# Kernel tuning notes

Measured on AMD Instinct MI355X. Metric: run time of the kernel, lower is better.

Reference implementation:

```python
import jax, jax.numpy as jnp
import numpy as np

N = 16384      # total atoms (8 proteins x ~2048)
E = 524288     # N * max_neighbors(32)
B = 8          # graphs
F_IN = 26      # 20 residue types + 6 atom types
D = 128        # node_dim
H = 256        # hidden_dim
OUT = 64       # output_dim
L = 4          # n_layers
N_RBF = 16
CUTOFF = 10.0


def setup_inputs() -> dict:
    key = jax.random.key(0)
    ks = jax.random.split(key, 24)
    s = 0.05
    inp = {
        "positions": jax.random.normal(ks[0], (N, 3), jnp.float32) * 10.0,
        "node_features": jax.random.normal(ks[1], (N, F_IN), jnp.float32),
        "edge_index": jax.random.randint(ks[2], (2, E), 0, N, jnp.int32),
        "batch": jnp.sort(jax.random.randint(ks[3], (N,), 0, B, jnp.int32)),
        # node embedding MLP
        "emb_W1": jax.random.normal(ks[4], (F_IN, D), jnp.float32) * s,
        "emb_b1": jnp.zeros((D,), jnp.float32),
        "emb_W2": jax.random.normal(ks[5], (D, D), jnp.float32) * s,
        "emb_b2": jnp.zeros((D,), jnp.float32),
        # per-layer message MLP: [2D + n_rbf] -> H -> D
        "msg_W1": jax.random.normal(ks[6], (L, 2 * D + N_RBF, H), jnp.float32) * s,
        "msg_b1": jnp.zeros((L, H), jnp.float32),
        "msg_W2": jax.random.normal(ks[7], (L, H, D), jnp.float32) * s,
        "msg_b2": jnp.zeros((L, D), jnp.float32),
        # per-layer update MLP: [2D] -> H -> D (residual)
        "upd_W1": jax.random.normal(ks[8], (L, 2 * D, H), jnp.float32) * s,
        "upd_b1": jnp.zeros((L, H), jnp.float32),
        "upd_W2": jax.random.normal(ks[9], (L, H, D), jnp.float32) * s,
        "upd_b2": jnp.zeros((L, D), jnp.float32),
        # readout MLP: D -> H -> OUT
        "r_W1": jax.random.normal(ks[10], (D, H), jnp.float32) * s,
        "r_b1": jnp.zeros((H,), jnp.float32),
        "r_W2": jax.random.normal(ks[11], (H, OUT), jnp.float32) * s,
        "r_b2": jnp.zeros((OUT,), jnp.float32),
    }
    return inp


def _mlp2(x, W1, b1, W2, b2):
    return jax.nn.silu(x @ W1 + b1) @ W2 + b2


def _edge_rbf(positions, src, dst):
    rel = positions[dst] - positions[src]                      # (E,3)
    d = jnp.sqrt(jnp.sum(rel * rel, axis=-1) + 1e-12)          # (E,)
    centers = jnp.linspace(0.0, CUTOFF, N_RBF, dtype=positions.dtype)
    width = CUTOFF / N_RBF
    rbf = jnp.exp(-((d[:, None] - centers) ** 2) / (2.0 * width * width))  # (E,n_rbf)
    env = 0.5 * (jnp.cos(jnp.pi * d / CUTOFF) + 1.0) * (d < CUTOFF)        # cosine cutoff
    return rbf * env[:, None]


def reference(positions, node_features, edge_index, batch,
              emb_W1, emb_b1, emb_W2, emb_b2,
              msg_W1, msg_b1, msg_W2, msg_b2,
              upd_W1, upd_b1, upd_W2, upd_b2,
              r_W1, r_b1, r_W2, r_b2):
    src, dst = edge_index[0], edge_index[1]
    h = _mlp2(node_features, emb_W1, emb_b1, emb_W2, emb_b2)   # (N,D)
    ef = _edge_rbf(positions, src, dst)                        # (E,n_rbf)
    for i in range(L):
        m_in = jnp.concatenate([h[src], h[dst], ef], axis=-1)  # (E,2D+n_rbf)
        m = _mlp2(m_in, msg_W1[i], msg_b1[i], msg_W2[i], msg_b2[i])  # (E,D)
        agg = jax.ops.segment_sum(m, dst, num_segments=N)      # (N,D)
        u_in = jnp.concatenate([h, agg], axis=-1)              # (N,2D)
        h = h + _mlp2(u_in, upd_W1[i], upd_b1[i], upd_W2[i], upd_b2[i])
    # mean readout per graph
    counts = jax.ops.segment_sum(jnp.ones((N,), h.dtype), batch, num_segments=B)
    g = jax.ops.segment_sum(h, batch, num_segments=B) / jnp.maximum(counts, 1.0)[:, None]
    return _mlp2(g, r_W1, r_b1, r_W2, r_b2)                    # (B,OUT)
```

## Files before the change

### kernel.cpp

```cpp
#include <hip/hip_runtime.h>
#include <math.h>

#define NATOMS 16384
#define NEDGES 524288
#define NLAYERS 4
#define TE 64

typedef __bf16 bf16x8 __attribute__((ext_vector_type(8)));
typedef __bf16 bf16x4 __attribute__((ext_vector_type(4)));
typedef __bf16 bf16x2 __attribute__((ext_vector_type(2)));
typedef float f32x4 __attribute__((ext_vector_type(4)));

__device__ __forceinline__ float silu_f(float x) {
  return x * __builtin_amdgcn_rcpf(1.0f + __expf(-x));
}

__global__ __launch_bounds__(1024) void scan_kernel(
    const int* __restrict__ counts, int* __restrict__ cursor,
    float* __restrict__ degf)
{
  __shared__ int s_tot[1024];
  int tid = threadIdx.x;
  int v[16];
  {
    const int4* cp = (const int4*)(counts + tid * 16);
    int4 a = cp[0], b = cp[1], c = cp[2], d = cp[3];
    v[0]=a.x; v[1]=a.y; v[2]=a.z; v[3]=a.w;
    v[4]=b.x; v[5]=b.y; v[6]=b.z; v[7]=b.w;
    v[8]=c.x; v[9]=c.y; v[10]=c.z; v[11]=c.w;
    v[12]=d.x; v[13]=d.y; v[14]=d.z; v[15]=d.w;
  }
  int tot = 0;
  #pragma unroll
  for (int i = 0; i < 16; i++) tot += v[i];
  s_tot[tid] = tot;
  __syncthreads();
  for (int off = 1; off < 1024; off <<= 1) {
    int t = (tid >= off) ? s_tot[tid - off] : 0;
    __syncthreads();
    s_tot[tid] += t;
    __syncthreads();
  }
  int run = s_tot[tid] - tot;
  #pragma unroll
  for (int i = 0; i < 16; i++) {
    cursor[tid * 16 + i] = run;
    degf[tid * 16 + i] = (float)v[i];
    run += v[i];
  }
}

__global__ __launch_bounds__(256) void scatter_rbf_kernel(
    const int* __restrict__ src, const int* __restrict__ dst,
    int* __restrict__ cursor, const float* __restrict__ pos,
    int* __restrict__ esrc, int* __restrict__ edst,
    __bf16* __restrict__ efb)
{
  int e = blockIdx.x * 256 + threadIdx.x;
  int s = src[e], d = dst[e];
  int p = atomicAdd(&cursor[d], 1);
  esrc[p] = s;
  edst[p] = d;
  float dx = pos[d * 3 + 0] - pos[s * 3 + 0];
  float dy = pos[d * 3 + 1] - pos[s * 3 + 1];
  float dz = pos[d * 3 + 2] - pos[s * 3 + 2];
  float dist = sqrtf(dx * dx + dy * dy + dz * dz + 1e-12f);
  float env = (dist < 10.0f)
                  ? 0.5f * (cosf(3.14159265358979f * dist * 0.1f) + 1.0f)
                  : 0.0f;
  bf16x8 o0, o1;
  #pragma unroll
  for (int i = 0; i < 16; i++) {
    float c = (10.0f / 15.0f) * (float)i;
    float t = dist - c;
    float v = env * __expf(-t * t * 1.28f);
    if (i < 8) o0[i] = (__bf16)v; else o1[i - 8] = (__bf16)v;
  }
  *(bf16x8*)(efb + (size_t)p * 16 + 0) = o0;
  *(bf16x8*)(efb + (size_t)p * 16 + 8) = o1;
}

#define NB_PL   50
#define NB_PREP (NB_PL * NLAYERS)
#define NB_HIST (NEDGES / 256)
#define NB_EMB  (NATOMS / 32)

__global__ __launch_bounds__(256) void front_kernel(
    const float* __restrict__ mW1, const float* __restrict__ mW2,
    const float* __restrict__ uW1, const float* __restrict__ uW2,
    const float* __restrict__ mb2,
    __bf16* __restrict__ W1at, __bf16* __restrict__ W1bt,
    __bf16* __restrict__ B2c, __bf16* __restrict__ uW1ft,
    __bf16* __restrict__ uW2t, float* __restrict__ b2u,
    const int* __restrict__ dstI, int* __restrict__ counts,
    const float* __restrict__ x, const float* __restrict__ eW1,
    const float* __restrict__ eb1, const float* __restrict__ eW2,
    const float* __restrict__ eb2, float* __restrict__ h,
    __bf16* __restrict__ hb)
{
  __shared__ __align__(16) char smem[19712];
  int bxf = blockIdx.x, tid = threadIdx.x;

  if (bxf < NB_PREP) {
    int l = bxf / NB_PL;
    int bx = bxf - l * NB_PL;
    if (bx < 16) {
      float (*tile)[65] = (float(*)[65])smem;
      int tt = bx & 7;
      int row0 = ((tt >> 2) * 64) + ((bx < 8) ? 0 : 128);
      int col0 = (tt & 3) * 64;
      const float* Sp = mW1 + (size_t)l * (272 * 256) + (size_t)row0 * 256 + col0;
      __bf16* Dq = ((bx < 8) ? W1at : W1bt) + (size_t)l * (256 * 128);
      int dro = (bx < 8) ? row0 : row0 - 128;
      int c = tid & 63, r4 = tid >> 6;
      #pragma unroll
      for (int i = 0; i < 16; i++)
        tile[r4 + i * 4][c] = Sp[(size_t)(r4 + i * 4) * 256 + c];
      __syncthreads();
      #pragma unroll
      for (int i = 0; i < 16; i++) {
        int dr = r4 + i * 4;
        Dq[(size_t)(col0 + dr) * 128 + dro + c] = (__bf16)tile[c][dr];
      }
    } else if (bx == 16) {
      float (*t3)[257] = (float(*)[257])smem;
      const float* Sp = mW1 + (size_t)l * (272 * 256) + 256 * 256;
      #pragma unroll
      for (int i = 0; i < 16; i++) t3[i][tid] = Sp[i * 256 + tid];
      __syncthreads();
      __bf16* Dp = B2c + (size_t)l * (256 * 32) + (size_t)tid * 32;
      #pragma unroll
      for (int g = 0; g < 4; g++) {
        bf16x8 o;
        #pragma unroll
        for (int j2 = 0; j2 < 8; j2++) {
          int k = g * 8 + j2;
          o[j2] = (__bf16)((k < 16) ? t3[k][tid] : 0.0f);
        }
        *(bf16x8*)(Dp + g * 8) = o;
      }
    } else if (bx < 25) {
      float (*tile)[65] = (float(*)[65])smem;
      int tt = bx - 17;
      int row0 = (tt >> 2) * 64;
      int col0 = (tt & 3) * 64;
      const float* Sp = uW1 + (size_t)l * 65536 + (size_t)row0 * 256 + col0;
      __bf16* Dq = uW1ft + (size_t)l * (256 * 384);
      int c = tid & 63, r4 = tid >> 6;
      #pragma unroll
      for (int i = 0; i < 16; i++)
        tile[r4 + i * 4][c] = Sp[(size_t)(r4 + i * 4) * 256 + c];
      __syncthreads();
      #pragma unroll
      for (int i = 0; i < 16; i++) {
        int dr = r4 + i * 4;
        Dq[(size_t)(col0 + dr) * 384 + row0 + c] = (__bf16)tile[c][dr];
      }
    } else if (bx < 41) {
      float (*sA)[128] = (float(*)[128])smem;
      int r0 = (bx - 25) * 16;
      const float* Ap = mW2 + (size_t)(l * 256 + r0) * 128;
      #pragma unroll
      for (int i = 0; i < 8; i++) {
        int idx = i * 256 + tid;
        ((float*)smem)[idx] = Ap[idx];
      }
      __syncthreads();
      const float* Bp = uW1 + (size_t)l * 65536 + 128 * 256 + tid;
      float acc[16];
      #pragma unroll
      for (int r = 0; r < 16; r++) acc[r] = 0.0f;
      for (int k = 0; k < 128; k++) {
        float b = Bp[(size_t)k * 256];
        #pragma unroll
        for (int r = 0; r < 16; r++) acc[r] += sA[r][k] * b;
      }
      __bf16* Dp = uW1ft + (size_t)l * (256 * 384) + (size_t)tid * 384 + 128 + r0;
      bf16x8 o0, o1;
      #pragma unroll
      for (int r = 0; r < 8; r++) { o0[r] = (__bf16)acc[r]; o1[r] = (__bf16)acc[8 + r]; }
      *(bf16x8*)Dp = o0;
      *(bf16x8*)(Dp + 8) = o1;
    } else if (bx < 49) {
      float (*tile)[65] = (float(*)[65])smem;
      int tt = bx - 41;
      int row0 = (tt >> 1) * 64;
      int col0 = (tt & 1) * 64;
      const float* Sp = uW2 + (size_t)l * (256 * 128) + (size_t)row0 * 128 + col0;
      __bf16* Dq = uW2t + (size_t)l * (128 * 256);
      int c = tid & 63, r4 = tid >> 6;
      #pragma unroll
      for (int i = 0; i < 16; i++)
        tile[r4 + i * 4][c] = Sp[(size_t)(r4 + i * 4) * 128 + c];
      __syncthreads();
      #pragma unroll
      for (int i = 0; i < 16; i++) {
        int dr = r4 + i * 4;
        Dq[(size_t)(col0 + dr) * 256 + row0 + c] = (__bf16)tile[c][dr];
      }
    } else {
      int cc = tid;
      float acc = 0.0f;
      for (int j2 = 0; j2 < 128; j2++)
        acc += mb2[l * 128 + j2] * uW1[(size_t)l * 65536 + (size_t)(128 + j2) * 256 + cc];
      b2u[l * 256 + cc] = acc;
    }
  } else if (bxf < NB_PREP + NB_HIST) {
    int e = (bxf - NB_PREP) * 256 + tid;
    atomicAdd(&counts[dstI[e]], 1);
  } else {
    int nb = bxf - (NB_PREP + NB_HIST);
    int n0e = nb * 32;
    float* xsf = (float*)smem;
    float (*hid2)[128] = (float(*)[128])(smem + 32 * 26 * 4);
    for (int i = tid; i < 32 * 26; i += 256)
      xsf[i] = x[(size_t)n0e * 26 + i];
    __syncthreads();
    int j = tid & 127, ns = tid >> 7;
    float a1[16];
    {
      float bb = eb1[j];
      #pragma unroll
      for (int i = 0; i < 16; i++) a1[i] = bb;
    }
    for (int k = 0; k < 26; k++) {
      float w = eW1[k * 128 + j];
      #pragma unroll
      for (int i = 0; i < 16; i++) a1[i] += xsf[(ns * 16 + i) * 26 + k] * w;
    }
    #pragma unroll
    for (int i = 0; i < 16; i++) hid2[ns * 16 + i][j] = silu_f(a1[i]);
    __syncthreads();
    float a2[16];
    {
      float bb = eb2[j];
      #pragma unroll
      for (int i = 0; i < 16; i++) a2[i] = bb;
    }
    for (int k = 0; k < 128; k++) {
      float w = eW2[k * 128 + j];
      #pragma unroll
      for (int i = 0; i < 16; i++) a2[i] += hid2[ns * 16 + i][k] * w;
    }
    #pragma unroll
    for (int i = 0; i < 16; i++) {
      int n = n0e + ns * 16 + i;
      h[(size_t)n * 128 + j] = a2[i];
      hb[(size_t)n * 128 + j] = (__bf16)a2[i];
    }
  }
}

__global__ __launch_bounds__(256) void zprep_kernel(
    const __bf16* __restrict__ hb, const float* __restrict__ b1,
    const __bf16* __restrict__ W1at, const __bf16* __restrict__ W1bt,
    __bf16* __restrict__ z1b, __bf16* __restrict__ z2b, float* __restrict__ aggH)
{
  __shared__ __bf16 s_n[64][136];
  int tid = threadIdx.x, n0 = blockIdx.x * 64;
  {
    int n = tid >> 2, t4 = tid & 3;
    const bf16x8* hr = (const bf16x8*)(hb + (size_t)(n0 + n) * 128);
    #pragma unroll
    for (int i = 0; i < 4; i++)
      *(bf16x8*)&s_n[n][t4 * 8 + 32 * i] = hr[t4 + 4 * i];
  }
  {
    float4 zz = make_float4(0.f, 0.f, 0.f, 0.f);
    float4* ap = (float4*)(aggH + (size_t)n0 * 256);
    for (int i = tid; i < 64 * 256 / 4; i += 256) ap[i] = zz;
  }
  __syncthreads();
  const int wv = tid >> 6, ln = tid & 63, lc = ln & 15, qd = ln >> 4;
  for (int cp = 0; cp < 2; cp++) {
    f32x4 aA[4][2], aB[4][2];
    #pragma unroll
    for (int nt = 0; nt < 2; nt++) {
      float bv = b1[cp * 128 + wv * 32 + nt * 16 + lc];
      #pragma unroll
      for (int mt = 0; mt < 4; mt++) {
        aA[mt][nt][0] = 0.f; aA[mt][nt][1] = 0.f;
        aA[mt][nt][2] = 0.f; aA[mt][nt][3] = 0.f;
        aB[mt][nt][0] = bv; aB[mt][nt][1] = bv;
        aB[mt][nt][2] = bv; aB[mt][nt][3] = bv;
      }
    }
    #pragma unroll
    for (int kt = 0; kt < 4; kt++) {
      bf16x8 af[4];
      #pragma unroll
      for (int mt = 0; mt < 4; mt++)
        af[mt] = *(const bf16x8*)&s_n[mt * 16 + lc][kt * 32 + qd * 8];
      bf16x8 bwA[2], bwB[2];
      #pragma unroll
      for (int nt = 0; nt < 2; nt++) {
        int c = cp * 128 + wv * 32 + nt * 16 + lc;
        bwA[nt] = *(const bf16x8*)(W1at + (size_t)c * 128 + kt * 32 + qd * 8);
        bwB[nt] = *(const bf16x8*)(W1bt + (size_t)c * 128 + kt * 32 + qd * 8);
      }
      #pragma unroll
      for (int mt = 0; mt < 4; mt++)
        #pragma unroll
        for (int nt = 0; nt < 2; nt++) {
          aA[mt][nt] = __builtin_amdgcn_mfma_f32_16x16x32_bf16(af[mt], bwA[nt], aA[mt][nt], 0, 0, 0);
          aB[mt][nt] = __builtin_amdgcn_mfma_f32_16x16x32_bf16(af[mt], bwB[nt], aB[mt][nt], 0, 0, 0);
        }
    }
    #pragma unroll
    for (int mt = 0; mt < 4; mt++)
      #pragma unroll
      for (int nt = 0; nt < 2; nt++) {
        int c = cp * 128 + wv * 32 + nt * 16 + lc;
        #pragma unroll
        for (int r = 0; r < 4; r++) {
          int n = n0 + mt * 16 + qd * 4 + r;
          z1b[(size_t)n * 256 + c] = (__bf16)aA[mt][nt][r];
          z2b[(size_t)n * 256 + c] = (__bf16)aB[mt][nt][r];
        }
      }
  }
}

__global__ __launch_bounds__(256, 8) void msg_mfma_kernel(
    const __bf16* __restrict__ z1b, const __bf16* __restrict__ z2b,
    const __bf16* __restrict__ efb,
    const int* __restrict__ esrc, const int* __restrict__ edst,
    const __bf16* __restrict__ B2c, float* __restrict__ aggH)
{
  __shared__ __align__(16) __bf16 s_hT[128][68];
  __shared__ __align__(16) __bf16 s_ef[TE][16];
  __shared__ int s_src[TE];
  __shared__ int s_dst[TE];
  __shared__ unsigned int s_mask[2];

  int tid = threadIdx.x, e0 = blockIdx.x * TE;

  if (tid < TE) {
    int d = edst[e0 + tid];
    s_dst[tid] = d;
    int dp = (tid == 0) ? (d ^ 1) : edst[e0 + tid - 1];
    unsigned long long mb = __ballot(d != dp);
    if (tid == 0) { s_mask[0] = (unsigned int)mb; s_mask[1] = (unsigned int)(mb >> 32); }
  } else if (tid < 2 * TE) {
    s_src[tid - TE] = esrc[e0 + tid - TE];
  }
  {
    int e = tid >> 2, t4 = tid & 3;
    if (t4 < 2)
      *(bf16x8*)&s_ef[e][t4 * 8] =
          *(const bf16x8*)(efb + (size_t)(e0 + e) * 16 + t4 * 8);
  }
  __syncthreads();

  const int wv = tid >> 6, ln = tid & 63, lc = ln & 15, qd = ln >> 4;

  bf16x8 bI;
  #pragma unroll
  for (int j = 0; j < 8; j++)
    bI[j] = (__bf16)((lc == (qd & 1) * 8 + j) ? 1.0f : 0.0f);

  const __bf16* pz[4];
  #pragma unroll
  for (int mt = 0; mt < 4; mt++) {
    int m = mt * 16 + lc;
    int row = (qd < 2) ? s_src[m] : s_dst[m];
    pz[mt] = ((qd < 2) ? z1b : z2b) + (size_t)row * 256 + (qd & 1) * 8;
  }

  bf16x8 aef[4];
  #pragma unroll
  for (int mt = 0; mt < 4; mt++)
    aef[mt] = *(const bf16x8*)&s_ef[mt * 16 + lc][(qd & 1) * 8];

  const int sj = tid & 127;
  const int srow0 = (tid >> 7) * 32;
  const unsigned int smask = __builtin_amdgcn_readfirstlane(s_mask[tid >> 7]);

  #pragma unroll
  for (int hf = 0; hf < 2; hf++) {
    if (hf) __syncthreads();

    #pragma unroll
    for (int nt = 0; nt < 2; nt++) {
      const int cb = hf * 128 + wv * 32 + nt * 16;
      bf16x8 bw = *(const bf16x8*)(B2c + (size_t)(cb + lc) * 32 + qd * 8);
      #pragma unroll
      for (int mt = 0; mt < 4; mt++) {
        bf16x8 az = *(const bf16x8*)(pz[mt] + cb);
        f32x4 z; z[0] = 0.f; z[1] = 0.f; z[2] = 0.f; z[3] = 0.f;
        f32x4 acc = __builtin_amdgcn_mfma_f32_16x16x32_bf16(az, bI, z, 0, 0, 0);
        acc = __builtin_amdgcn_mfma_f32_16x16x32_bf16(aef[mt], bw, acc, 0, 0, 0);
        bf16x4 pv;
        pv[0] = (__bf16)silu_f(acc[0]); pv[1] = (__bf16)silu_f(acc[1]);
        pv[2] = (__bf16)silu_f(acc[2]); pv[3] = (__bf16)silu_f(acc[3]);
        *(bf16x4*)&s_hT[wv * 32 + nt * 16 + lc][mt * 16 + qd * 4] = pv;
      }
    }
    __syncthreads();

    {
      const int gcol = hf * 128 + sj;
      float acc = 0.0f;
      int cur = s_dst[srow0];
      #pragma unroll
      for (int i = 0; i < 32; i += 4) {
        unsigned int bm = (smask >> i) & 0xFu;
        if (i == 0) bm &= 0xEu;
        bf16x4 p = *(const bf16x4*)&s_hT[sj][srow0 + i];
        if (bm == 0u) {
          acc += ((float)p[0] + (float)p[1]) + ((float)p[2] + (float)p[3]);
        } else {
          #pragma unroll
          for (int r = 0; r < 4; r++) {
            if ((bm >> r) & 1u) {
              atomicAdd(&aggH[(size_t)cur * 256 + gcol], acc);
              acc = 0.0f; cur = s_dst[srow0 + i + r];
            }
            acc += (float)p[r];
          }
        }
      }
      atomicAdd(&aggH[(size_t)cur * 256 + gcol], acc);
    }
  }
}

__global__ __launch_bounds__(512, 2) void upd_mfma_kernel(
    float* __restrict__ h, __bf16* __restrict__ hb,
    float* __restrict__ aggH, const float* __restrict__ degf,
    const __bf16* __restrict__ uW1ft, const float* __restrict__ b1,
    const float* __restrict__ b2u,
    const __bf16* __restrict__ uW2t, const float* __restrict__ b2,
    int do_z, const float* __restrict__ nb1,
    const __bf16* __restrict__ nW1at, const __bf16* __restrict__ nW1bt,
    __bf16* __restrict__ z1b, __bf16* __restrict__ z2b)
{
  __shared__ __bf16 s_u[64][392];
  __shared__ __bf16 s_uh[64][264];
  int tid = threadIdx.x, n0 = blockIdx.x * 64;
  {
    int n = tid >> 3, t8 = tid & 7;
    const bf16x8* hr = (const bf16x8*)(hb + (size_t)(n0 + n) * 128);
    #pragma unroll
    for (int i = 0; i < 2; i++)
      *(bf16x8*)&s_u[n][t8 * 8 + 64 * i] = hr[t8 + 8 * i];
    const float* sr = aggH + (size_t)(n0 + n) * 256;
    #pragma unroll
    for (int i = 0; i < 4; i++) {
      int col = t8 * 8 + i * 64;
      float4 a = *(const float4*)(sr + col);
      float4 b = *(const float4*)(sr + col + 4);
      bf16x8 o;
      o[0] = (__bf16)a.x; o[1] = (__bf16)a.y; o[2] = (__bf16)a.z; o[3] = (__bf16)a.w;
      o[4] = (__bf16)b.x; o[5] = (__bf16)b.y; o[6] = (__bf16)b.z; o[7] = (__bf16)b.w;
      *(bf16x8*)&s_u[n][128 + col] = o;
    }
  }
  __syncthreads();
  const int wv = tid >> 6, ln = tid & 63, lc = ln & 15, qd = ln >> 4;

  float dg[4][4];
  #pragma unroll
  for (int mt = 0; mt < 4; mt++)
    #pragma unroll
    for (int r = 0; r < 4; r++)
      dg[mt][r] = degf[n0 + mt * 16 + qd * 4 + r];

  {
    f32x4 acc1[4][2];
    #pragma unroll
    for (int nt = 0; nt < 2; nt++) {
      int c = wv * 32 + nt * 16 + lc;
      float bv = b1[c];
      float b2uv = b2u[c];
      #pragma unroll
      for (int mt = 0; mt < 4; mt++)
        #pragma unroll
        for (int r = 0; r < 4; r++)
          acc1[mt][nt][r] = bv + dg[mt][r] * b2uv;
    }
    #pragma unroll
    for (int kt = 0; kt < 12; kt++) {
      bf16x8 af[4];
      #pragma unroll
      for (int mt = 0; mt < 4; mt++)
        af[mt] = *(const bf16x8*)&s_u[mt * 16 + lc][kt * 32 + qd * 8];
      bf16x8 bw[2];
      #pragma unroll
      for (int nt = 0; nt < 2; nt++)
        bw[nt] = *(const bf16x8*)(uW1ft +
                 (size_t)(wv * 32 + nt * 16 + lc) * 384 + kt * 32 + qd * 8);
      #pragma unroll
      for (int mt = 0; mt < 4; mt++)
        #pragma unroll
        for (int nt = 0; nt < 2; nt++)
          acc1[mt][nt] = __builtin_amdgcn_mfma_f32_16x16x32_bf16(af[mt], bw[nt], acc1[mt][nt], 0, 0, 0);
    }
    #pragma unroll
    for (int mt = 0; mt < 4; mt++)
      #pragma unroll
      for (int nt = 0; nt < 2; nt++) {
        int cc = wv * 32 + nt * 16 + lc;
        #pragma unroll
        for (int r = 0; r < 4; r++)
          s_uh[mt * 16 + qd * 4 + r][cc] = (__bf16)silu_f(acc1[mt][nt][r]);
      }
  }
  __syncthreads();

  const int ow = wv * 16 + lc;
  f32x4 acc2[4];
  {
    float bv = b2[ow];
    #pragma unroll
    for (int mt = 0; mt < 4; mt++) {
      acc2[mt][0] = bv; acc2[mt][1] = bv; acc2[mt][2] = bv; acc2[mt][3] = bv;
    }
  }
  #pragma unroll
  for (int kt = 0; kt < 8; kt++) {
    bf16x8 a2[4];
    #pragma unroll
    for (int mt = 0; mt < 4; mt++)
      a2[mt] = *(const bf16x8*)&s_uh[mt * 16 + lc][kt * 32 + qd * 8];
    bf16x8 b2w = *(const bf16x8*)(uW2t + (size_t)ow * 256 + kt * 32 + qd * 8);
    #pragma unroll
    for (int mt = 0; mt < 4; mt++)
      acc2[mt] = __builtin_amdgcn_mfma_f32_16x16x32_bf16(a2[mt], b2w, acc2[mt], 0, 0, 0);
  }

  #pragma unroll
  for (int mt = 0; mt < 4; mt++)
    #pragma unroll
    for (int r = 0; r < 4; r++) {
      int n = n0 + mt * 16 + qd * 4 + r;
      float v = h[(size_t)n * 128 + ow] + acc2[mt][r];
      h[(size_t)n * 128 + ow] = v;
      hb[(size_t)n * 128 + ow] = (__bf16)v;
    }

  if (do_z) {
    __syncthreads();
    {
      float4 zz = make_float4(0.f, 0.f, 0.f, 0.f);
      float4* ap = (float4*)(aggH + (size_t)n0 * 256);
      for (int i = tid; i < 64 * 256 / 4; i += 512) ap[i] = zz;
      int n = tid >> 3, t8 = tid & 7;
      const bf16x8* hr = (const bf16x8*)(hb + (size_t)(n0 + n) * 128);
      #pragma unroll
      for (int i = 0; i < 2; i++)
        *(bf16x8*)&s_u[n][t8 * 8 + 64 * i] = hr[t8 + 8 * i];
    }
    __syncthreads();
    f32x4 aA[4][2], aB[4][2];
    #pragma unroll
    for (int nt = 0; nt < 2; nt++) {
      float bv = nb1[wv * 32 + nt * 16 + lc];
      #pragma unroll
      for (int mt = 0; mt < 4; mt++) {
        aA[mt][nt][0] = 0.f; aA[mt][nt][1] = 0.f;
        aA[mt][nt][2] = 0.f; aA[mt][nt][3] = 0.f;
        aB[mt][nt][0] = bv; aB[mt][nt][1] = bv;
        aB[mt][nt][2] = bv; aB[mt][nt][3] = bv;
      }
    }
    #pragma unroll
    for (int kt = 0; kt < 4; kt++) {
      bf16x8 af[4];
      #pragma unroll
      for (int mt = 0; mt < 4; mt++)
        af[mt] = *(const bf16x8*)&s_u[mt * 16 + lc][kt * 32 + qd * 8];
      bf16x8 bwA[2], bwB[2];
      #pragma unroll
      for (int nt = 0; nt < 2; nt++) {
        int c = wv * 32 + nt * 16 + lc;
        bwA[nt] = *(const bf16x8*)(nW1at + (size_t)c * 128 + kt * 32 + qd * 8);
        bwB[nt] = *(const bf16x8*)(nW1bt + (size_t)c * 128 + kt * 32 + qd * 8);
      }
      #pragma unroll
      for (int mt = 0; mt < 4; mt++)
        #pragma unroll
        for (int nt = 0; nt < 2; nt++) {
          aA[mt][nt] = __builtin_amdgcn_mfma_f32_16x16x32_bf16(af[mt], bwA[nt], aA[mt][nt], 0, 0, 0);
          aB[mt][nt] = __builtin_amdgcn_mfma_f32_16x16x32_bf16(af[mt], bwB[nt], aB[mt][nt], 0, 0, 0);
        }
    }
    #pragma unroll
    for (int mt = 0; mt < 4; mt++)
      #pragma unroll
      for (int nt = 0; nt < 2; nt++) {
        int c = wv * 32 + nt * 16 + lc;
        #pragma unroll
        for (int r = 0; r < 4; r++) {
          int n = n0 + mt * 16 + qd * 4 + r;
          z1b[(size_t)n * 256 + c] = (__bf16)aA[mt][nt][r];
          z2b[(size_t)n * 256 + c] = (__bf16)aB[mt][nt][r];
        }
      }
  }
}

__global__ __launch_bounds__(128) void readout_sum_kernel(
    const float* __restrict__ h, const int* __restrict__ batch,
    float* __restrict__ gsum, float* __restrict__ gcnt)
{
  int j = threadIdx.x;
  int n0 = blockIdx.x * 128;
  float acc = 0.f, cacc = 0.f;
  int cur = batch[n0];
  for (int i = 0; i < 128; i++) {
    int b = batch[n0 + i];
    if (b != cur) {
      atomicAdd(&gsum[cur * 128 + j], acc);
      if (j == 0) atomicAdd(&gcnt[cur], cacc);
      acc = 0.f; cacc = 0.f; cur = b;
    }
    acc += h[(size_t)(n0 + i) * 128 + j];
    cacc += 1.f;
  }
  atomicAdd(&gsum[cur * 128 + j], acc);
  if (j == 0) atomicAdd(&gcnt[cur], cacc);
}

__global__ __launch_bounds__(256) void readout_mlp_kernel(
    const float* __restrict__ gsum, const float* __restrict__ gcnt,
    const float* __restrict__ W1, const float* __restrict__ b1,
    const float* __restrict__ W2, const float* __restrict__ b2,
    float* __restrict__ out)
{
  __shared__ float g[8][128];
  __shared__ float hid[8][256];
  int tid = threadIdx.x;
  for (int i = tid; i < 8 * 128; i += 256) {
    int b = i >> 7, c = i & 127;
    g[b][c] = gsum[i] / fmaxf(gcnt[b], 1.0f);
  }
  __syncthreads();
  {
    float bb = b1[tid];
    float a[8];
    #pragma unroll
    for (int b = 0; b < 8; b++) a[b] = bb;
    for (int k = 0; k < 128; k++) {
      float w = W1[k * 256 + tid];
      #pragma unroll
      for (int b = 0; b < 8; b++) a[b] += g[b][k] * w;
    }
    #pragma unroll
    for (int b = 0; b < 8; b++) hid[b][tid] = silu_f(a[b]);
  }
  __syncthreads();
  int j = tid & 63, bg = tid >> 6;
  float a0 = b2[j], a1 = b2[j];
  for (int k = 0; k < 256; k++) {
    float w = W2[k * 64 + j];
    a0 += hid[bg * 2 + 0][k] * w;
    a1 += hid[bg * 2 + 1][k] * w;
  }
  out[(bg * 2 + 0) * 64 + j] = a0;
  out[(bg * 2 + 1) * 64 + j] = a1;
}

extern "C" void kernel_launch(void* const* d_in, const int* in_sizes, int n_in,
                              void* d_out, int out_size, void* d_ws, size_t ws_size,
                              hipStream_t stream) {
  const float* pos   = (const float*)d_in[0];
  const float* xfeat = (const float*)d_in[1];
  const int*   eidx  = (const int*)d_in[2];
  const int*   batch = (const int*)d_in[3];
  const float* eW1 = (const float*)d_in[4];
  const float* eb1 = (const float*)d_in[5];
  const float* eW2 = (const float*)d_in[6];
  const float* eb2 = (const float*)d_in[7];
  const float* mW1 = (const float*)d_in[8];
  const float* mb1 = (const float*)d_in[9];
  const float* mW2 = (const float*)d_in[10];
  const float* mb2 = (const float*)d_in[11];
  const float* uW1 = (const float*)d_in[12];
  const float* ub1 = (const float*)d_in[13];
  const float* uW2 = (const float*)d_in[14];
  const float* ub2 = (const float*)d_in[15];
  const float* rW1 = (const float*)d_in[16];
  const float* rb1 = (const float*)d_in[17];
  const float* rW2 = (const float*)d_in[18];
  const float* rb2 = (const float*)d_in[19];

  const int* srcI = eidx;
  const int* dstI = eidx + NEDGES;

  char* base = (char*)d_ws;
  float* h    = (float*)base;  base += (size_t)NATOMS * 128 * 4;
  float* aggH = (float*)base;  base += (size_t)NATOMS * 256 * 4;
  __bf16* z1b = (__bf16*)base; base += (size_t)NATOMS * 256 * 2;
  __bf16* z2b = (__bf16*)base; base += (size_t)NATOMS * 256 * 2;
  __bf16* hb  = (__bf16*)base; base += (size_t)NATOMS * 128 * 2;
  __bf16* efb = (__bf16*)base; base += (size_t)NEDGES * 16 * 2;
  __bf16* W1at = (__bf16*)base; base += (size_t)NLAYERS * 256 * 128 * 2;
  __bf16* W1bt = (__bf16*)base; base += (size_t)NLAYERS * 256 * 128 * 2;
  __bf16* B2c  = (__bf16*)base; base += (size_t)NLAYERS * 256 * 32 * 2;
  __bf16* uW1ft = (__bf16*)base; base += (size_t)NLAYERS * 256 * 384 * 2;
  __bf16* uW2t = (__bf16*)base; base += (size_t)NLAYERS * 128 * 256 * 2;
  float* b2u  = (float*)base;  base += (size_t)NLAYERS * 256 * 4;
  float* degf = (float*)base;  base += (size_t)NATOMS * 4;
  float* gsum = (float*)base;  base += 8 * 128 * 4;
  float* gcnt = (float*)base;  base += 8 * 4;
  int* counts = (int*)base;    base += (size_t)NATOMS * 4;
  int* cursor = (int*)base;    base += (size_t)NATOMS * 4;
  int* esrc   = (int*)base;    base += (size_t)NEDGES * 4;
  int* edst   = (int*)base;    base += (size_t)NEDGES * 4;

  hipMemsetAsync(counts, 0, NATOMS * sizeof(int), stream);

  front_kernel<<<NB_PREP + NB_HIST + NB_EMB, 256, 0, stream>>>(
      mW1, mW2, uW1, uW2, mb2, W1at, W1bt, B2c, uW1ft, uW2t, b2u,
      dstI, counts, xfeat, eW1, eb1, eW2, eb2, h, hb);

  scan_kernel<<<1, 1024, 0, stream>>>(counts, cursor, degf);
  scatter_rbf_kernel<<<NEDGES / 256, 256, 0, stream>>>(
      srcI, dstI, cursor, pos, esrc, edst, efb);

  zprep_kernel<<<NATOMS / 64, 256, 0, stream>>>(
      hb, mb1, W1at, W1bt, z1b, z2b, aggH);

  for (int l = 0; l < NLAYERS; l++) {
    int ln = (l < NLAYERS - 1) ? (l + 1) : l;
    msg_mfma_kernel<<<NEDGES / TE, 256, 0, stream>>>(
        z1b, z2b, efb, esrc, edst,
        B2c + (size_t)l * 256 * 32, aggH);
    upd_mfma_kernel<<<NATOMS / 64, 512, 0, stream>>>(
        h, hb, aggH, degf,
        uW1ft + (size_t)l * 256 * 384, ub1 + (size_t)l * 256,
        b2u + (size_t)l * 256,
        uW2t + (size_t)l * 128 * 256, ub2 + (size_t)l * 128,
        (l < NLAYERS - 1) ? 1 : 0,
        mb1 + (size_t)ln * 256,
        W1at + (size_t)ln * 256 * 128, W1bt + (size_t)ln * 256 * 128,
        z1b, z2b);
  }

  hipMemsetAsync(gsum, 0, (8 * 128 + 8) * sizeof(float), stream);
  readout_sum_kernel<<<NATOMS / 128, 128, 0, stream>>>(h, batch, gsum, gcnt);
  readout_mlp_kernel<<<1, 256, 0, stream>>>(gsum, gcnt, rW1, rb1, rW2, rb2,
                                            (float*)d_out);
}
```

Before: 578.6 us.

## Reduce message MLP outputs in registers instead of staging through LDS

The message kernel no longer writes the SiLU outputs to a shared-memory transpose buffer followed by a segmented scan. Each 16-row MFMA tile is now reduced directly in registers with cross-lane shuffles when all rows share one destination, and atomics go straight to global memory. Otherwise it falls back to per-lane-quad segmented atomics. This removes the LDS buffer and two block barriers per half, but may issue more global atomics when destinations change within a tile.

```diff
diff --git a/kernel.cpp b/kernel.cpp
--- a/kernel.cpp
+++ b/kernel.cpp
@@ -327,7 +327,6 @@
     const int* __restrict__ esrc, const int* __restrict__ edst,
     const __bf16* __restrict__ B2c, float* __restrict__ aggH)
 {
-  __shared__ __align__(16) __bf16 s_hT[128][68];
   __shared__ __align__(16) __bf16 s_ef[TE][16];
   __shared__ int s_src[TE];
   __shared__ int s_dst[TE];
@@ -354,6 +353,9 @@
 
   const int wv = tid >> 6, ln = tid & 63, lc = ln & 15, qd = ln >> 4;
 
+  const unsigned int mlo = __builtin_amdgcn_readfirstlane(s_mask[0]);
+  const unsigned int mhi = __builtin_amdgcn_readfirstlane(s_mask[1]);
+
   bf16x8 bI;
   #pragma unroll
   for (int j = 0; j < 8; j++)
@@ -372,55 +374,53 @@
   for (int mt = 0; mt < 4; mt++)
     aef[mt] = *(const bf16x8*)&s_ef[mt * 16 + lc][(qd & 1) * 8];
 
-  const int sj = tid & 127;
-  const int srow0 = (tid >> 7) * 32;
-  const unsigned int smask = __builtin_amdgcn_readfirstlane(s_mask[tid >> 7]);
+  int dw[4];
+  #pragma unroll
+  for (int mt = 0; mt < 4; mt++) dw[mt] = s_dst[mt * 16];
+  const int row0q = qd * 4;
 
   #pragma unroll
   for (int hf = 0; hf < 2; hf++) {
-    if (hf) __syncthreads();
-
     #pragma unroll
     for (int nt = 0; nt < 2; nt++) {
       const int cb = hf * 128 + wv * 32 + nt * 16;
       bf16x8 bw = *(const bf16x8*)(B2c + (size_t)(cb + lc) * 32 + qd * 8);
+      const int col = cb + lc;
       #pragma unroll
       for (int mt = 0; mt < 4; mt++) {
         bf16x8 az = *(const bf16x8*)(pz[mt] + cb);
         f32x4 z; z[0] = 0.f; z[1] = 0.f; z[2] = 0.f; z[3] = 0.f;
         f32x4 acc = __builtin_amdgcn_mfma_f32_16x16x32_bf16(az, bI, z, 0, 0, 0);
         acc = __builtin_amdgcn_mfma_f32_16x16x32_bf16(aef[mt], bw, acc, 0, 0, 0);
-        bf16x4 pv;
-        pv[0] = (__bf16)silu_f(acc[0]); pv[1] = (__bf16)silu_f(acc[1]);
-        pv[2] = (__bf16)silu_f(acc[2]); pv[3] = (__bf16)silu_f(acc[3]);
-        *(bf16x4*)&s_hT[wv * 32 + nt * 16 + lc][mt * 16 + qd * 4] = pv;
-      }
-    }
-    __syncthreads();
-
-    {
-      const int gcol = hf * 128 + sj;
-      float acc = 0.0f;
-      int cur = s_dst[srow0];
-      #pragma unroll
-      for (int i = 0; i < 32; i += 4) {
-        unsigned int bm = (smask >> i) & 0xFu;
-        if (i == 0) bm &= 0xEu;
-        bf16x4 p = *(const bf16x4*)&s_hT[sj][srow0 + i];
-        if (bm == 0u) {
-          acc += ((float)p[0] + (float)p[1]) + ((float)p[2] + (float)p[3]);
+        float p0 = silu_f(acc[0]), p1 = silu_f(acc[1]);
+        float p2 = silu_f(acc[2]), p3 = silu_f(acc[3]);
+        unsigned int wbits =
+            (((mt < 2) ? mlo : mhi) >> ((mt & 1) * 16 + 1)) & 0x7FFFu;
+        if (wbits == 0u) {
+          float s4 = (p0 + p1) + (p2 + p3);
+          s4 += __shfl_xor(s4, 16, 64);
+          s4 += __shfl_xor(s4, 32, 64);
+          if (qd == 0)
+            atomicAdd(&aggH[(size_t)dw[mt] * 256 + col], s4);
         } else {
+          int row0 = mt * 16 + row0q;
+          float a2 = 0.0f;
+          int cur = s_dst[row0];
+          float pv[4] = {p0, p1, p2, p3};
           #pragma unroll
           for (int r = 0; r < 4; r++) {
-            if ((bm >> r) & 1u) {
-              atomicAdd(&aggH[(size_t)cur * 256 + gcol], acc);
-              acc = 0.0f; cur = s_dst[srow0 + i + r];
+            int row = row0 + r;
+            bool b = (row < 32) ? ((mlo >> row) & 1u)
+                                : ((mhi >> (row - 32)) & 1u);
+            if (r > 0 && b) {
+              atomicAdd(&aggH[(size_t)cur * 256 + col], a2);
+              a2 = 0.0f; cur = s_dst[row];
             }
-            acc += (float)p[r];
+            a2 += pv[r];
           }
+          atomicAdd(&aggH[(size_t)cur * 256 + col], a2);
         }
       }
-      atomicAdd(&aggH[(size_t)cur * 256 + gcol], acc);
     }
   }
 }
```

Measured after the change: 1.038 ms. 1.79x slower.

## Retile update kernel to 16-node blocks of 256 threads for more parallelism

Applied to the files above, without the earlier changes.

The node update MLP kernel now processes 16 nodes per block with 4 waves instead of 64 nodes with 8 waves, launching 1024 blocks instead of 256. Each wave now covers a wider slice of output columns with a single M-tile. The aim is to fill all compute units on the GPU, since 256 blocks underuse the device. The cost is that weight matrices are reloaded from global/L2 four times more often per node, and each B fragment now feeds only one MFMA.

```diff
diff --git a/kernel.cpp b/kernel.cpp
--- a/kernel.cpp
+++ b/kernel.cpp
@@ -425,7 +425,7 @@
   }
 }
 
-__global__ __launch_bounds__(512, 2) void upd_mfma_kernel(
+__global__ __launch_bounds__(256, 4) void upd_mfma_kernel(
     float* __restrict__ h, __bf16* __restrict__ hb,
     float* __restrict__ aggH, const float* __restrict__ degf,
     const __bf16* __restrict__ uW1ft, const float* __restrict__ b1,
@@ -435,19 +435,17 @@
     const __bf16* __restrict__ nW1at, const __bf16* __restrict__ nW1bt,
     __bf16* __restrict__ z1b, __bf16* __restrict__ z2b)
 {
-  __shared__ __bf16 s_u[64][392];
-  __shared__ __bf16 s_uh[64][264];
-  int tid = threadIdx.x, n0 = blockIdx.x * 64;
+  __shared__ __bf16 s_u[16][392];
+  __shared__ __bf16 s_uh[16][264];
+  int tid = threadIdx.x, n0 = blockIdx.x * 16;
   {
-    int n = tid >> 3, t8 = tid & 7;
+    int n = tid >> 4, t16 = tid & 15;
     const bf16x8* hr = (const bf16x8*)(hb + (size_t)(n0 + n) * 128);
-    #pragma unroll
-    for (int i = 0; i < 2; i++)
-      *(bf16x8*)&s_u[n][t8 * 8 + 64 * i] = hr[t8 + 8 * i];
+    *(bf16x8*)&s_u[n][t16 * 8] = hr[t16];
     const float* sr = aggH + (size_t)(n0 + n) * 256;
     #pragma unroll
-    for (int i = 0; i < 4; i++) {
-      int col = t8 * 8 + i * 64;
+    for (int i = 0; i < 2; i++) {
+      int col = t16 * 8 + i * 128;
       float4 a = *(const float4*)(sr + col);
       float4 b = *(const float4*)(sr + col + 4);
       bf16x8 o;
@@ -459,144 +457,112 @@
   __syncthreads();
   const int wv = tid >> 6, ln = tid & 63, lc = ln & 15, qd = ln >> 4;
 
-  float dg[4][4];
-  #pragma unroll
-  for (int mt = 0; mt < 4; mt++)
-    #pragma unroll
-    for (int r = 0; r < 4; r++)
-      dg[mt][r] = degf[n0 + mt * 16 + qd * 4 + r];
+  float dg[4];
+  #pragma unroll
+  for (int r = 0; r < 4; r++)
+    dg[r] = degf[n0 + qd * 4 + r];
 
   {
-    f32x4 acc1[4][2];
-    #pragma unroll
-    for (int nt = 0; nt < 2; nt++) {
-      int c = wv * 32 + nt * 16 + lc;
+    f32x4 acc1[4];
+    #pragma unroll
+    for (int nt = 0; nt < 4; nt++) {
+      int c = wv * 64 + nt * 16 + lc;
       float bv = b1[c];
       float b2uv = b2u[c];
       #pragma unroll
-      for (int mt = 0; mt < 4; mt++)
-        #pragma unroll
-        for (int r = 0; r < 4; r++)
-          acc1[mt][nt][r] = bv + dg[mt][r] * b2uv;
+      for (int r = 0; r < 4; r++)
+        acc1[nt][r] = bv + dg[r] * b2uv;
     }
     #pragma unroll
     for (int kt = 0; kt < 12; kt++) {
-      bf16x8 af[4];
-      #pragma unroll
-      for (int mt = 0; mt < 4; mt++)
-        af[mt] = *(const bf16x8*)&s_u[mt * 16 + lc][kt * 32 + qd * 8];
-      bf16x8 bw[2];
-      #pragma unroll
-      for (int nt = 0; nt < 2; nt++)
-        bw[nt] = *(const bf16x8*)(uW1ft +
-                 (size_t)(wv * 32 + nt * 16 + lc) * 384 + kt * 32 + qd * 8);
-      #pragma unroll
-      for (int mt = 0; mt < 4; mt++)
-        #pragma unroll
-        for (int nt = 0; nt < 2; nt++)
-          acc1[mt][nt] = __builtin_amdgcn_mfma_f32_16x16x32_bf16(af[mt], bw[nt], acc1[mt][nt], 0, 0, 0);
-    }
-    #pragma unroll
-    for (int mt = 0; mt < 4; mt++)
-      #pragma unroll
-      for (int nt = 0; nt < 2; nt++) {
-        int cc = wv * 32 + nt * 16 + lc;
-        #pragma unroll
-        for (int r = 0; r < 4; r++)
-          s_uh[mt * 16 + qd * 4 + r][cc] = (__bf16)silu_f(acc1[mt][nt][r]);
-      }
+      bf16x8 af = *(const bf16x8*)&s_u[lc][kt * 32 + qd * 8];
+      #pragma unroll
+      for (int nt = 0; nt < 4; nt++) {
+        bf16x8 bw = *(const bf16x8*)(uW1ft +
+                 (size_t)(wv * 64 + nt * 16 + lc) * 384 + kt * 32 + qd * 8);
+        acc1[nt] = __builtin_amdgcn_mfma_f32_16x16x32_bf16(af, bw, acc1[nt], 0, 0, 0);
+      }
+    }
+    #pragma unroll
+    for (int nt = 0; nt < 4; nt++) {
+      int cc = wv * 64 + nt * 16 + lc;
+      #pragma unroll
+      for (int r = 0; r < 4; r++)
+        s_uh[qd * 4 + r][cc] = (__bf16)silu_f(acc1[nt][r]);
+    }
   }
   __syncthreads();
 
-  const int ow = wv * 16 + lc;
-  f32x4 acc2[4];
-  {
-    float bv = b2[ow];
-    #pragma unroll
-    for (int mt = 0; mt < 4; mt++) {
-      acc2[mt][0] = bv; acc2[mt][1] = bv; acc2[mt][2] = bv; acc2[mt][3] = bv;
-    }
+  f32x4 acc2[2];
+  #pragma unroll
+  for (int nt = 0; nt < 2; nt++) {
+    float bv = b2[wv * 32 + nt * 16 + lc];
+    acc2[nt][0] = bv; acc2[nt][1] = bv; acc2[nt][2] = bv; acc2[nt][3] = bv;
   }
   #pragma unroll
   for (int kt = 0; kt < 8; kt++) {
-    bf16x8 a2[4];
-    #pragma unroll
-    for (int mt = 0; mt < 4; mt++)
-      a2[mt] = *(const bf16x8*)&s_uh[mt * 16 + lc][kt * 32 + qd * 8];
-    bf16x8 b2w = *(const bf16x8*)(uW2t + (size_t)ow * 256 + kt * 32 + qd * 8);
-    #pragma unroll
-    for (int mt = 0; mt < 4; mt++)
-      acc2[mt] = __builtin_amdgcn_mfma_f32_16x16x32_bf16(a2[mt], b2w, acc2[mt], 0, 0, 0);
-  }
-
-  #pragma unroll
-  for (int mt = 0; mt < 4; mt++)
+    bf16x8 a2 = *(const bf16x8*)&s_uh[lc][kt * 32 + qd * 8];
+    #pragma unroll
+    for (int nt = 0; nt < 2; nt++) {
+      bf16x8 b2w = *(const bf16x8*)(uW2t +
+               (size_t)(wv * 32 + nt * 16 + lc) * 256 + kt * 32 + qd * 8);
+      acc2[nt] = __builtin_amdgcn_mfma_f32_16x16x32_bf16(a2, b2w, acc2[nt], 0, 0, 0);
+    }
+  }
+
+  #pragma unroll
+  for (int nt = 0; nt < 2; nt++) {
+    int ow = wv * 32 + nt * 16 + lc;
     #pragma unroll
     for (int r = 0; r < 4; r++) {
-      int n = n0 + mt * 16 + qd * 4 + r;
-      float v = h[(size_t)n * 128 + ow] + acc2[mt][r];
+      int n = n0 + qd * 4 + r;
+      float v = h[(size_t)n * 128 + ow] + acc2[nt][r];
       h[(size_t)n * 128 + ow] = v;
       hb[(size_t)n * 128 + ow] = (__bf16)v;
     }
+  }
 
   if (do_z) {
     __syncthreads();
     {
+      int n = tid >> 4, t16 = tid & 15;
+      const bf16x8* hr = (const bf16x8*)(hb + (size_t)(n0 + n) * 128);
+      *(bf16x8*)&s_u[n][t16 * 8] = hr[t16];
       float4 zz = make_float4(0.f, 0.f, 0.f, 0.f);
       float4* ap = (float4*)(aggH + (size_t)n0 * 256);
-      for (int i = tid; i < 64 * 256 / 4; i += 512) ap[i] = zz;
-      int n = tid >> 3, t8 = tid & 7;
-      const bf16x8* hr = (const bf16x8*)(hb + (size_t)(n0 + n) * 128);
-      #pragma unroll
-      for (int i = 0; i < 2; i++)
-        *(bf16x8*)&s_u[n][t8 * 8 + 64 * i] = hr[t8 + 8 * i];
+      #pragma unroll
+      for (int i = 0; i < 4; i++) ap[tid + i * 256] = zz;
     }
     __syncthreads();
-    f32x4 aA[4][2], aB[4][2];
-    #pragma unroll
-    for (int nt = 0; nt < 2; nt++) {
-      float bv = nb1[wv * 32 + nt * 16 + lc];
-      #pragma unroll
-      for (int mt = 0; mt < 4; mt++) {
-        aA[mt][nt][0] = 0.f; aA[mt][nt][1] = 0.f;
-        aA[mt][nt][2] = 0.f; aA[mt][nt][3] = 0.f;
-        aB[mt][nt][0] = bv; aB[mt][nt][1] = bv;
-        aB[mt][nt][2] = bv; aB[mt][nt][3] = bv;
-      }
+    f32x4 aA[4], aB[4];
+    #pragma unroll
+    for (int nt = 0; nt < 4; nt++) {
+      float bv = nb1[wv * 64 + nt * 16 + lc];
+      aA[nt][0] = 0.f; aA[nt][1] = 0.f; aA[nt][2] = 0.f; aA[nt][3] = 0.f;
+      aB[nt][0] = bv; aB[nt][1] = bv; aB[nt][2] = bv; aB[nt][3] = bv;
     }
     #pragma unroll
     for (int kt = 0; kt < 4; kt++) {
-      bf16x8 af[4];
-      #pragma unroll
-      for (int mt = 0; mt < 4; mt++)
-        af[mt] = *(const bf16x8*)&s_u[mt * 16 + lc][kt * 32 + qd * 8];
-      bf16x8 bwA[2], bwB[2];
-      #pragma unroll
-      for (int nt = 0; nt < 2; nt++) {
-        int c = wv * 32 + nt * 16 + lc;
-        bwA[nt] = *(const bf16x8*)(nW1at + (size_t)c * 128 + kt * 32 + qd * 8);
-        bwB[nt] = *(const bf16x8*)(nW1bt + (size_t)c * 128 + kt * 32 + qd * 8);
-      }
-      #pragma unroll
-      for (int mt = 0; mt < 4; mt++)
-        #pragma unroll
-        for (int nt = 0; nt < 2; nt++) {
-          aA[mt][nt] = __builtin_amdgcn_mfma_f32_16x16x32_bf16(af[mt], bwA[nt], aA[mt][nt], 0, 0, 0);
-          aB[mt][nt] = __builtin_amdgcn_mfma_f32_16x16x32_bf16(af[mt], bwB[nt], aB[mt][nt], 0, 0, 0);
-        }
-    }
-    #pragma unroll
-    for (int mt = 0; mt < 4; mt++)
-      #pragma unroll
-      for (int nt = 0; nt < 2; nt++) {
-        int c = wv * 32 + nt * 16 + lc;
-        #pragma unroll
-        for (int r = 0; r < 4; r++) {
-          int n = n0 + mt * 16 + qd * 4 + r;
-          z1b[(size_t)n * 256 + c] = (__bf16)aA[mt][nt][r];
-          z2b[(size_t)n * 256 + c] = (__bf16)aB[mt][nt][r];
-        }
-      }
+      bf16x8 af = *(const bf16x8*)&s_u[lc][kt * 32 + qd * 8];
+      #pragma unroll
+      for (int nt = 0; nt < 4; nt++) {
+        int c = wv * 64 + nt * 16 + lc;
+        bf16x8 bwA = *(const bf16x8*)(nW1at + (size_t)c * 128 + kt * 32 + qd * 8);
+        bf16x8 bwB = *(const bf16x8*)(nW1bt + (size_t)c * 128 + kt * 32 + qd * 8);
+        aA[nt] = __builtin_amdgcn_mfma_f32_16x16x32_bf16(af, bwA, aA[nt], 0, 0, 0);
+        aB[nt] = __builtin_amdgcn_mfma_f32_16x16x32_bf16(af, bwB, aB[nt], 0, 0, 0);
+      }
+    }
+    #pragma unroll
+    for (int nt = 0; nt < 4; nt++) {
+      int c = wv * 64 + nt * 16 + lc;
+      #pragma unroll
+      for (int r = 0; r < 4; r++) {
+        int n = n0 + qd * 4 + r;
+        z1b[(size_t)n * 256 + c] = (__bf16)aA[nt][r];
+        z2b[(size_t)n * 256 + c] = (__bf16)aB[nt][r];
+      }
+    }
   }
 }
 
@@ -727,7 +693,7 @@
     msg_mfma_kernel<<<NEDGES / TE, 256, 0, stream>>>(
         z1b, z2b, efb, esrc, edst,
         B2c + (size_t)l * 256 * 32, aggH);
-    upd_mfma_kernel<<<NATOMS / 64, 512, 0, stream>>>(
+    upd_mfma_kernel<<<NATOMS / 16, 256, 0, stream>>>(
         h, hb, aggH, degf,
         uW1ft + (size_t)l * 256 * 384, ub1 + (size_t)l * 256,
         b2u + (size_t)l * 256,
```

After: 671.6 us. 1.16x slower.

## Reduce edge messages per destination segment in LDS before global atomics

Applied to the files above, without the earlier changes.

Replaces the transposed bf16 staging buffer and serial per-column segmented scan with per-segment float accumulators in shared memory. Each edge tile computes segment ids by ballot/popcount, MFMA outputs are atomically added into LDS rows indexed by segment (one combined add when all four rows share a segment), and then one global atomic per segment per column is issued. This aims to remove the serial scan loop and one barrier, but adds LDS atomics, a 16KB float buffer, and a multi-pass fallback when a tile has more than 16 destination segments.

```diff
diff --git a/kernel.cpp b/kernel.cpp
--- a/kernel.cpp
+++ b/kernel.cpp
@@ -327,11 +327,13 @@
     const int* __restrict__ esrc, const int* __restrict__ edst,
     const __bf16* __restrict__ B2c, float* __restrict__ aggH)
 {
-  __shared__ __align__(16) __bf16 s_hT[128][68];
+  __shared__ float s_agg[16][256];
   __shared__ __align__(16) __bf16 s_ef[TE][16];
   __shared__ int s_src[TE];
   __shared__ int s_dst[TE];
-  __shared__ unsigned int s_mask[2];
+  __shared__ int s_dseg[TE];
+  __shared__ unsigned char s_seg[TE];
+  __shared__ int s_nseg;
 
   int tid = threadIdx.x, e0 = blockIdx.x * TE;
 
@@ -340,7 +342,11 @@
     s_dst[tid] = d;
     int dp = (tid == 0) ? (d ^ 1) : edst[e0 + tid - 1];
     unsigned long long mb = __ballot(d != dp);
-    if (tid == 0) { s_mask[0] = (unsigned int)mb; s_mask[1] = (unsigned int)(mb >> 32); }
+    unsigned long long below = mb & (~0ull >> (63 - tid));
+    int seg = (int)__popcll(below) - 1;
+    s_seg[tid] = (unsigned char)seg;
+    if (d != dp) s_dseg[seg] = d;
+    if (tid == 0) s_nseg = (int)__popcll(mb);
   } else if (tid < 2 * TE) {
     s_src[tid - TE] = esrc[e0 + tid - TE];
   }
@@ -350,9 +356,12 @@
       *(bf16x8*)&s_ef[e][t4 * 8] =
           *(const bf16x8*)(efb + (size_t)(e0 + e) * 16 + t4 * 8);
   }
+  #pragma unroll
+  for (int r = 0; r < 16; r++) s_agg[r][tid] = 0.0f;
   __syncthreads();
 
   const int wv = tid >> 6, ln = tid & 63, lc = ln & 15, qd = ln >> 4;
+  const int nseg = __builtin_amdgcn_readfirstlane(s_nseg);
 
   bf16x8 bI;
   #pragma unroll
@@ -372,55 +381,80 @@
   for (int mt = 0; mt < 4; mt++)
     aef[mt] = *(const bf16x8*)&s_ef[mt * 16 + lc][(qd & 1) * 8];
 
-  const int sj = tid & 127;
-  const int srow0 = (tid >> 7) * 32;
-  const unsigned int smask = __builtin_amdgcn_readfirstlane(s_mask[tid >> 7]);
-
-  #pragma unroll
-  for (int hf = 0; hf < 2; hf++) {
-    if (hf) __syncthreads();
-
-    #pragma unroll
-    for (int nt = 0; nt < 2; nt++) {
-      const int cb = hf * 128 + wv * 32 + nt * 16;
-      bf16x8 bw = *(const bf16x8*)(B2c + (size_t)(cb + lc) * 32 + qd * 8);
-      #pragma unroll
-      for (int mt = 0; mt < 4; mt++) {
-        bf16x8 az = *(const bf16x8*)(pz[mt] + cb);
-        f32x4 z; z[0] = 0.f; z[1] = 0.f; z[2] = 0.f; z[3] = 0.f;
-        f32x4 acc = __builtin_amdgcn_mfma_f32_16x16x32_bf16(az, bI, z, 0, 0, 0);
-        acc = __builtin_amdgcn_mfma_f32_16x16x32_bf16(aef[mt], bw, acc, 0, 0, 0);
-        bf16x4 pv;
-        pv[0] = (__bf16)silu_f(acc[0]); pv[1] = (__bf16)silu_f(acc[1]);
-        pv[2] = (__bf16)silu_f(acc[2]); pv[3] = (__bf16)silu_f(acc[3]);
-        *(bf16x4*)&s_hT[wv * 32 + nt * 16 + lc][mt * 16 + qd * 4] = pv;
-      }
-    }
-    __syncthreads();
-
-    {
-      const int gcol = hf * 128 + sj;
-      float acc = 0.0f;
-      int cur = s_dst[srow0];
-      #pragma unroll
-      for (int i = 0; i < 32; i += 4) {
-        unsigned int bm = (smask >> i) & 0xFu;
-        if (i == 0) bm &= 0xEu;
-        bf16x4 p = *(const bf16x4*)&s_hT[sj][srow0 + i];
-        if (bm == 0u) {
-          acc += ((float)p[0] + (float)p[1]) + ((float)p[2] + (float)p[3]);
-        } else {
-          #pragma unroll
-          for (int r = 0; r < 4; r++) {
-            if ((bm >> r) & 1u) {
-              atomicAdd(&aggH[(size_t)cur * 256 + gcol], acc);
-              acc = 0.0f; cur = s_dst[srow0 + i + r];
-            }
-            acc += (float)p[r];
+  unsigned int sw[4];
+  int sg0[4];
+  bool eqm[4];
+  #pragma unroll
+  for (int mt = 0; mt < 4; mt++) {
+    sw[mt] = *(const unsigned int*)&s_seg[mt * 16 + qd * 4];
+    sg0[mt] = (int)(sw[mt] & 255u);
+    eqm[mt] = (sw[mt] == (sw[mt] & 255u) * 0x01010101u);
+  }
+
+  if (nseg <= 16) {
+    #pragma unroll
+    for (int hf = 0; hf < 2; hf++) {
+      #pragma unroll
+      for (int nt = 0; nt < 2; nt++) {
+        const int cb = hf * 128 + wv * 32 + nt * 16;
+        bf16x8 bw = *(const bf16x8*)(B2c + (size_t)(cb + lc) * 32 + qd * 8);
+        const int col = cb + lc;
+        #pragma unroll
+        for (int mt = 0; mt < 4; mt++) {
+          bf16x8 az = *(const bf16x8*)(pz[mt] + cb);
+          f32x4 z; z[0] = 0.f; z[1] = 0.f; z[2] = 0.f; z[3] = 0.f;
+          f32x4 acc = __builtin_amdgcn_mfma_f32_16x16x32_bf16(az, bI, z, 0, 0, 0);
+          acc = __builtin_amdgcn_mfma_f32_16x16x32_bf16(aef[mt], bw, acc, 0, 0, 0);
+          float p0 = silu_f(acc[0]), p1 = silu_f(acc[1]);
+          float p2 = silu_f(acc[2]), p3 = silu_f(acc[3]);
+          if (eqm[mt]) {
+            atomicAdd(&s_agg[sg0[mt]][col], (p0 + p1) + (p2 + p3));
+          } else {
+            atomicAdd(&s_agg[(sw[mt] >> 0) & 255][col], p0);
+            atomicAdd(&s_agg[(sw[mt] >> 8) & 255][col], p1);
+            atomicAdd(&s_agg[(sw[mt] >> 16) & 255][col], p2);
+            atomicAdd(&s_agg[(sw[mt] >> 24) & 255][col], p3);
           }
         }
       }
-      atomicAdd(&aggH[(size_t)cur * 256 + gcol], acc);
+    }
+    __syncthreads();
+    for (int r = 0; r < nseg; r++)
+      atomicAdd(&aggH[(size_t)s_dseg[r] * 256 + tid], s_agg[r][tid]);
+  } else {
+    for (int ps = 0; ps < nseg; ps += 16) {
+      if (ps > 0) {
+        __syncthreads();
+        #pragma unroll
+        for (int r = 0; r < 16; r++) s_agg[r][tid] = 0.0f;
+        __syncthreads();
+      }
+      #pragma unroll
+      for (int hf = 0; hf < 2; hf++) {
+        #pragma unroll
+        for (int nt = 0; nt < 2; nt++) {
+          const int cb = hf * 128 + wv * 32 + nt * 16;
+          bf16x8 bw = *(const bf16x8*)(B2c + (size_t)(cb + lc) * 32 + qd * 8);
+          const int col = cb + lc;
+          #pragma unroll
+          for (int mt = 0; mt < 4; mt++) {
+            bf16x8 az = *(const bf16x8*)(pz[mt] + cb);
+            f32x4 z; z[0] = 0.f; z[1] = 0.f; z[2] = 0.f; z[3] = 0.f;
+            f32x4 acc = __builtin_amdgcn_mfma_f32_16x16x32_bf16(az, bI, z, 0, 0, 0);
+            acc = __builtin_amdgcn_mfma_f32_16x16x32_bf16(aef[mt], bw, acc, 0, 0, 0);
+            #pragma unroll
+            for (int r = 0; r < 4; r++) {
+              int s = (int)((sw[mt] >> (8 * r)) & 255u) - ps;
+              if ((unsigned)s < 16u)
+                atomicAdd(&s_agg[s][col], silu_f(acc[r]));
+            }
+          }
+        }
+      }
+      __syncthreads();
+      int rows = nseg - ps; if (rows > 16) rows = 16;
+      for (int r = 0; r < rows; r++)
+        atomicAdd(&aggH[(size_t)s_dseg[ps + r] * 256 + tid], s_agg[r][tid]);
     }
   }
 }
```

Measured after the change: 1.284 ms. +121.9%, slower.
